# Kernel optimization log

Measured on AMD Instinct MI355X. Metric: run time of the kernel, lower is better.

Reference implementation:

```python
import jax, jax.numpy as jnp
import numpy as np

N_STEPS = 3            # n_internal_steps
USE_CURRENT_ACTIVS = True
LEAKY_SLOPE = 0.01     # F.leaky_relu default


def _apply_act(x, ids):
    # per-node activation lookup: 0=identity 1=leaky_relu 2=relu 3=sigmoid 4=tanh
    return jnp.select(
        [ids == 0, ids == 1, ids == 2, ids == 3],
        [x,
         jnp.where(x >= 0, x, LEAKY_SLOPE * x),
         jnp.maximum(x, jnp.zeros((), x.dtype)),
         jax.nn.sigmoid(x)],
        jnp.tanh(x))


def setup_inputs() -> dict:
    key = jax.random.key(0)
    ks = jax.random.split(key, 14)
    B, NI, NH, NO = 1, 4096, 8192, 2048
    s = 0.02  # keep recurrent dynamics stable
    return {
        "inputs": jax.random.normal(ks[0], (B, NI), jnp.float32),
        "W_i2h": jax.random.normal(ks[1], (NH, NI), jnp.float32) * s,
        "W_h2h": jax.random.normal(ks[2], (NH, NH), jnp.float32) * s,
        "W_o2h": jax.random.normal(ks[3], (NH, NO), jnp.float32) * s,
        "W_i2o": jax.random.normal(ks[4], (NO, NI), jnp.float32) * s,
        "W_h2o": jax.random.normal(ks[5], (NO, NH), jnp.float32) * s,
        "W_o2o": jax.random.normal(ks[6], (NO, NO), jnp.float32) * s,
        "hidden_responses": jax.random.uniform(ks[7], (NH,), jnp.float32, 0.5, 1.5),
        "hidden_biases": jax.random.normal(ks[8], (NH,), jnp.float32) * 0.1,
        "output_responses": jax.random.uniform(ks[9], (NO,), jnp.float32, 0.5, 1.5),
        "output_biases": jax.random.normal(ks[10], (NO,), jnp.float32) * 0.1,
        "activs0": jnp.zeros((B, NH), jnp.float32),
        "outputs0": jnp.zeros((B, NO), jnp.float32),
        "hidden_act_ids": jax.random.randint(ks[11], (NH,), 0, 5, jnp.int32),
        "output_act_ids": jax.random.randint(ks[12], (NO,), 0, 5, jnp.int32),
    }


def reference(inputs, W_i2h, W_h2h, W_o2h, W_i2o, W_h2o, W_o2o,
              hidden_responses, hidden_biases, output_responses, output_biases,
              activs0, outputs0, hidden_act_ids, output_act_ids):
    activs = activs0          # (B, NH) recurrent hidden state
    outputs = outputs0        # (B, NO) recurrent output state
    activs_for_output = activs
    for _ in range(N_STEPS):
        pre = hidden_responses * (inputs @ W_i2h.T
                                  + activs @ W_h2h.T
                                  + outputs @ W_o2h.T) + hidden_biases
        activs = _apply_act(pre, hidden_act_ids[None, :])
    if USE_CURRENT_ACTIVS:
        activs_for_output = activs
    out_in = inputs @ W_i2o.T + outputs @ W_o2o.T + activs_for_output @ W_h2o.T
    pre_out = output_responses * out_in + output_biases
    return _apply_act(pre_out, output_act_ids[None, :])
```

## Files before the change

### kernel.cpp

```cpp
#include <hip/hip_runtime.h>

#define NI 4096
#define NH 8192
#define NO 2048

__device__ __forceinline__ float apply_act(float x, int id) {
    switch (id) {
        case 0:  return x;
        case 1:  return x >= 0.f ? x : 0.01f * x;
        case 2:  return fmaxf(x, 0.f);
        case 3:  return 1.f / (1.f + expf(-x));
        default: return tanhf(x);
    }
}

__device__ __forceinline__ float wave_dot(const float* __restrict__ Wrow,
                                          const float* __restrict__ x,
                                          int K, int lane) {
    const float4* __restrict__ W4 = (const float4*)Wrow;
    const float4* __restrict__ x4 = (const float4*)x;
    float acc = 0.f;
    const int n4 = K >> 2;
    #pragma unroll 4
    for (int i = lane; i < n4; i += 64) {
        float4 w = W4[i];
        float4 v = x4[i];
        acc = fmaf(w.x, v.x, acc);
        acc = fmaf(w.y, v.y, acc);
        acc = fmaf(w.z, v.z, acc);
        acc = fmaf(w.w, v.w, acc);
    }
    #pragma unroll
    for (int off = 32; off; off >>= 1) acc += __shfl_xor(acc, off, 64);
    return acc;
}

__global__ __launch_bounds__(256) void k_flags(const float* __restrict__ xin,
                                               const float* __restrict__ a0,
                                               const float* __restrict__ o0,
                                               int* __restrict__ flags) {
    int tid = blockIdx.x * 256 + threadIdx.x;
    int stride = gridDim.x * 256;
    int f0 = 0, f1 = 0, f2 = 0;
    for (int i = tid; i < NI; i += stride) f0 |= (xin[i] != 0.f);
    for (int i = tid; i < NH; i += stride) f1 |= (a0[i]  != 0.f);
    for (int i = tid; i < NO; i += stride) f2 |= (o0[i]  != 0.f);
    if (f0) atomicOr(flags + 0, 1);
    if (f1) atomicOr(flags + 1, 1);
    if (f2) atomicOr(flags + 2, 1);
}

__global__ __launch_bounds__(256) void k_const_h(const float* __restrict__ W_i2h,
                                                 const float* __restrict__ W_o2h,
                                                 const float* __restrict__ xin,
                                                 const float* __restrict__ o0,
                                                 const int* __restrict__ flags,
                                                 float* __restrict__ c_h) {
    int wave = threadIdx.x >> 6;
    int lane = threadIdx.x & 63;
    int m = blockIdx.x * 4 + wave;
    float dot = 0.f;
    if (flags[0]) dot += wave_dot(W_i2h + (size_t)m * NI, xin, NI, lane);
    if (flags[2]) dot += wave_dot(W_o2h + (size_t)m * NO, o0,  NO, lane);
    if (lane == 0) c_h[m] = dot;
}

__global__ __launch_bounds__(256) void k_step(const float* __restrict__ W_h2h,
                                              const float* __restrict__ x,
                                              const float* __restrict__ c_h,
                                              const float* __restrict__ resp,
                                              const float* __restrict__ bias,
                                              const int* __restrict__ ids,
                                              const int* __restrict__ flag,
                                              float* __restrict__ out) {
    int wave = threadIdx.x >> 6;
    int lane = threadIdx.x & 63;
    int m = blockIdx.x * 4 + wave;
    float dot = 0.f;
    if (!flag || flag[0]) dot = wave_dot(W_h2h + (size_t)m * NH, x, NH, lane);
    if (lane == 0) {
        float pre = fmaf(resp[m], c_h[m] + dot, bias[m]);
        out[m] = apply_act(pre, ids[m]);
    }
}

__global__ __launch_bounds__(256) void k_final(const float* __restrict__ W_i2o,
                                               const float* __restrict__ W_o2o,
                                               const float* __restrict__ W_h2o,
                                               const float* __restrict__ xin,
                                               const float* __restrict__ o0,
                                               const float* __restrict__ act,
                                               const float* __restrict__ resp,
                                               const float* __restrict__ bias,
                                               const int* __restrict__ ids,
                                               const int* __restrict__ flags,
                                               float* __restrict__ out) {
    int wave = threadIdx.x >> 6;
    int lane = threadIdx.x & 63;
    int m = blockIdx.x * 4 + wave;
    float dot = wave_dot(W_h2o + (size_t)m * NH, act, NH, lane);
    if (flags[0]) dot += wave_dot(W_i2o + (size_t)m * NI, xin, NI, lane);
    if (flags[2]) dot += wave_dot(W_o2o + (size_t)m * NO, o0,  NO, lane);
    if (lane == 0) {
        float pre = fmaf(resp[m], dot, bias[m]);
        out[m] = apply_act(pre, ids[m]);
    }
}

extern "C" void kernel_launch(void* const* d_in, const int* in_sizes, int n_in,
                              void* d_out, int out_size, void* d_ws, size_t ws_size,
                              hipStream_t stream) {
    const float* inputs   = (const float*)d_in[0];
    const float* W_i2h    = (const float*)d_in[1];
    const float* W_h2h    = (const float*)d_in[2];
    const float* W_o2h    = (const float*)d_in[3];
    const float* W_i2o    = (const float*)d_in[4];
    const float* W_h2o    = (const float*)d_in[5];
    const float* W_o2o    = (const float*)d_in[6];
    const float* h_resp   = (const float*)d_in[7];
    const float* h_bias   = (const float*)d_in[8];
    const float* o_resp   = (const float*)d_in[9];
    const float* o_bias   = (const float*)d_in[10];
    const float* activs0  = (const float*)d_in[11];
    const float* outputs0 = (const float*)d_in[12];
    const int*   h_ids    = (const int*)d_in[13];
    const int*   o_ids    = (const int*)d_in[14];

    float* ws    = (float*)d_ws;
    float* c_h   = ws;
    float* act_a = ws + NH;
    float* act_b = ws + 2 * NH;
    int*   flags = (int*)(ws + 3 * NH);

    hipMemsetAsync(flags, 0, 3 * sizeof(int), stream);
    k_flags<<<32, 256, 0, stream>>>(inputs, activs0, outputs0, flags);

    k_const_h<<<NH / 4, 256, 0, stream>>>(W_i2h, W_o2h, inputs, outputs0, flags, c_h);

    k_step<<<NH / 4, 256, 0, stream>>>(W_h2h, activs0, c_h, h_resp, h_bias, h_ids,
                                       flags + 1, act_a);
    k_step<<<NH / 4, 256, 0, stream>>>(W_h2h, act_a, c_h, h_resp, h_bias, h_ids,
                                       nullptr, act_b);
    k_step<<<NH / 4, 256, 0, stream>>>(W_h2h, act_b, c_h, h_resp, h_bias, h_ids,
                                       nullptr, act_a);

    k_final<<<NO / 4, 256, 0, stream>>>(W_i2o, W_o2o, W_h2o, inputs, outputs0, act_a,
                                        o_resp, o_bias, o_ids, flags, (float*)d_out);
}
```

Baseline: 145.5 us.

## Fuse first hidden step into constant kernel, add nontemporal loads and reversed step order

Merges the constant input/output contribution and the first recurrent step into one kernel, which removes one launch and one dependent pass. Streaming-only weights (W_i2h, W_o2h, output weights) now use nontemporal loads so they are less likely to evict W_h2h from the last-level cache. The second step walks rows in reverse so the W_h2h rows most recently touched by the previous step are read first while still cached. The flag kernel becomes a single block that reduces in shared memory, which drops the memset.

```diff
diff --git a/kernel.cpp b/kernel.cpp
--- a/kernel.cpp
+++ b/kernel.cpp
@@ -3,6 +3,8 @@
 #define NI 4096
 #define NH 8192
 #define NO 2048
+
+typedef float f4 __attribute__((ext_vector_type(4)));
 
 __device__ __forceinline__ float apply_act(float x, int id) {
     switch (id) {
@@ -14,17 +16,18 @@
     }
 }
 
+template <bool NT>
 __device__ __forceinline__ float wave_dot(const float* __restrict__ Wrow,
                                           const float* __restrict__ x,
                                           int K, int lane) {
-    const float4* __restrict__ W4 = (const float4*)Wrow;
-    const float4* __restrict__ x4 = (const float4*)x;
+    const f4* __restrict__ W4 = (const f4*)Wrow;
+    const f4* __restrict__ x4 = (const f4*)x;
     float acc = 0.f;
     const int n4 = K >> 2;
     #pragma unroll 4
     for (int i = lane; i < n4; i += 64) {
-        float4 w = W4[i];
-        float4 v = x4[i];
+        f4 w = NT ? __builtin_nontemporal_load(W4 + i) : W4[i];
+        f4 v = x4[i];
         acc = fmaf(w.x, v.x, acc);
         acc = fmaf(w.y, v.y, acc);
         acc = fmaf(w.z, v.z, acc);
@@ -39,45 +42,60 @@
                                                const float* __restrict__ a0,
                                                const float* __restrict__ o0,
                                                int* __restrict__ flags) {
-    int tid = blockIdx.x * 256 + threadIdx.x;
-    int stride = gridDim.x * 256;
+    __shared__ int s[3];
+    int t = threadIdx.x;
+    if (t < 3) s[t] = 0;
+    __syncthreads();
     int f0 = 0, f1 = 0, f2 = 0;
-    for (int i = tid; i < NI; i += stride) f0 |= (xin[i] != 0.f);
-    for (int i = tid; i < NH; i += stride) f1 |= (a0[i]  != 0.f);
-    for (int i = tid; i < NO; i += stride) f2 |= (o0[i]  != 0.f);
-    if (f0) atomicOr(flags + 0, 1);
-    if (f1) atomicOr(flags + 1, 1);
-    if (f2) atomicOr(flags + 2, 1);
+    for (int i = t; i < NI; i += 256) f0 |= (xin[i] != 0.f);
+    for (int i = t; i < NH; i += 256) f1 |= (a0[i]  != 0.f);
+    for (int i = t; i < NO; i += 256) f2 |= (o0[i]  != 0.f);
+    if (f0) atomicOr(&s[0], 1);
+    if (f1) atomicOr(&s[1], 1);
+    if (f2) atomicOr(&s[2], 1);
+    __syncthreads();
+    if (t < 3) flags[t] = s[t];
 }
 
-__global__ __launch_bounds__(256) void k_const_h(const float* __restrict__ W_i2h,
-                                                 const float* __restrict__ W_o2h,
-                                                 const float* __restrict__ xin,
-                                                 const float* __restrict__ o0,
-                                                 const int* __restrict__ flags,
-                                                 float* __restrict__ c_h) {
+__global__ __launch_bounds__(256) void k_h_init(const float* __restrict__ W_i2h,
+                                                const float* __restrict__ W_o2h,
+                                                const float* __restrict__ W_h2h,
+                                                const float* __restrict__ xin,
+                                                const float* __restrict__ o0,
+                                                const float* __restrict__ a0,
+                                                const float* __restrict__ resp,
+                                                const float* __restrict__ bias,
+                                                const int* __restrict__ ids,
+                                                const int* __restrict__ flags,
+                                                float* __restrict__ c_h,
+                                                float* __restrict__ act_a) {
     int wave = threadIdx.x >> 6;
     int lane = threadIdx.x & 63;
     int m = blockIdx.x * 4 + wave;
-    float dot = 0.f;
-    if (flags[0]) dot += wave_dot(W_i2h + (size_t)m * NI, xin, NI, lane);
-    if (flags[2]) dot += wave_dot(W_o2h + (size_t)m * NO, o0,  NO, lane);
-    if (lane == 0) c_h[m] = dot;
+    float c = 0.f;
+    if (flags[0]) c += wave_dot<true>(W_i2h + (size_t)m * NI, xin, NI, lane);
+    if (flags[2]) c += wave_dot<true>(W_o2h + (size_t)m * NO, o0,  NO, lane);
+    float d = 0.f;
+    if (flags[1]) d = wave_dot<false>(W_h2h + (size_t)m * NH, a0, NH, lane);
+    if (lane == 0) {
+        c_h[m] = c;
+        act_a[m] = apply_act(fmaf(resp[m], c + d, bias[m]), ids[m]);
+    }
 }
 
+template <int REV>
 __global__ __launch_bounds__(256) void k_step(const float* __restrict__ W_h2h,
                                               const float* __restrict__ x,
                                               const float* __restrict__ c_h,
                                               const float* __restrict__ resp,
                                               const float* __restrict__ bias,
                                               const int* __restrict__ ids,
-                                              const int* __restrict__ flag,
                                               float* __restrict__ out) {
     int wave = threadIdx.x >> 6;
     int lane = threadIdx.x & 63;
     int m = blockIdx.x * 4 + wave;
-    float dot = 0.f;
-    if (!flag || flag[0]) dot = wave_dot(W_h2h + (size_t)m * NH, x, NH, lane);
+    if (REV) m = (NH - 1) - m;
+    float dot = wave_dot<false>(W_h2h + (size_t)m * NH, x, NH, lane);
     if (lane == 0) {
         float pre = fmaf(resp[m], c_h[m] + dot, bias[m]);
         out[m] = apply_act(pre, ids[m]);
@@ -98,9 +116,9 @@
     int wave = threadIdx.x >> 6;
     int lane = threadIdx.x & 63;
     int m = blockIdx.x * 4 + wave;
-    float dot = wave_dot(W_h2o + (size_t)m * NH, act, NH, lane);
-    if (flags[0]) dot += wave_dot(W_i2o + (size_t)m * NI, xin, NI, lane);
-    if (flags[2]) dot += wave_dot(W_o2o + (size_t)m * NO, o0,  NO, lane);
+    float dot = wave_dot<true>(W_h2o + (size_t)m * NH, act, NH, lane);
+    if (flags[0]) dot += wave_dot<true>(W_i2o + (size_t)m * NI, xin, NI, lane);
+    if (flags[2]) dot += wave_dot<true>(W_o2o + (size_t)m * NO, o0,  NO, lane);
     if (lane == 0) {
         float pre = fmaf(resp[m], dot, bias[m]);
         out[m] = apply_act(pre, ids[m]);
@@ -132,17 +150,15 @@
     float* act_b = ws + 2 * NH;
     int*   flags = (int*)(ws + 3 * NH);
 
-    hipMemsetAsync(flags, 0, 3 * sizeof(int), stream);
-    k_flags<<<32, 256, 0, stream>>>(inputs, activs0, outputs0, flags);
+    k_flags<<<1, 256, 0, stream>>>(inputs, activs0, outputs0, flags);
 
-    k_const_h<<<NH / 4, 256, 0, stream>>>(W_i2h, W_o2h, inputs, outputs0, flags, c_h);
-
-    k_step<<<NH / 4, 256, 0, stream>>>(W_h2h, activs0, c_h, h_resp, h_bias, h_ids,
-                                       flags + 1, act_a);
-    k_step<<<NH / 4, 256, 0, stream>>>(W_h2h, act_a, c_h, h_resp, h_bias, h_ids,
-                                       nullptr, act_b);
-    k_step<<<NH / 4, 256, 0, stream>>>(W_h2h, act_b, c_h, h_resp, h_bias, h_ids,
-                                       nullptr, act_a);
+    k_h_init<<<NH / 4, 256, 0, stream>>>(W_i2h, W_o2h, W_h2h, inputs, outputs0,
+                                         activs0, h_resp, h_bias, h_ids, flags,
+                                         c_h, act_a);
+    k_step<0><<<NH / 4, 256, 0, stream>>>(W_h2h, act_a, c_h, h_resp, h_bias, h_ids,
+                                          act_b);
+    k_step<1><<<NH / 4, 256, 0, stream>>>(W_h2h, act_b, c_h, h_resp, h_bias, h_ids,
+                                          act_a);
 
     k_final<<<NO / 4, 256, 0, stream>>>(W_i2o, W_o2o, W_h2o, inputs, outputs0, act_a,
                                         o_resp, o_bias, o_ids, flags, (float*)d_out);
```

After: 134.4 us. 1.08x faster.
